# Kernel optimization log

Hardware: AMD Instinct MI355X
Metric: run time of the kernel (lower is better)

Reference implementation:

```python
import jax, jax.numpy as jnp
import numpy as np

# Model dims (match init_kwargs)
B, L, C = 4, 4096, 1024   # batch, seq_len, dim
M = 128                   # memory_dim
P = 4                     # n_persistent
S = 64                    # segment_size
H = 8                     # num_heads in nn.MultiheadAttention


def _ln(x, g, b, eps=1e-5):
    mu = jnp.mean(x, -1, keepdims=True)
    var = jnp.mean((x - mu) ** 2, -1, keepdims=True)
    return (x - mu) * jax.lax.rsqrt(var + eps) * g + b


def setup_inputs() -> dict:
    key = jax.random.key(0)
    ks = jax.random.split(key, 16)
    def n(k, shape, s=0.02):
        return jax.random.normal(k, shape, jnp.float32) * s
    return {
        "x": jax.random.normal(ks[0], (B, L, C), jnp.float32),
        "persistent_memory": n(ks[1], (1, P, C)),
        "Wq": n(ks[2], (C, C)),            # query_proj (no bias)
        "Wk": n(ks[3], (C, C)),            # key_proj (no bias)
        "Wv": n(ks[4], (C, C)),            # value_proj (no bias)
        # NeuralMemoryModule.memory_net: Linear(C->M), SiLU, LN(M), Linear(M->M), LN(M)
        "mem_W1": n(ks[5], (M, C)), "mem_b1": jnp.zeros((M,)),
        "mem_ln1_g": jnp.ones((M,)), "mem_ln1_b": jnp.zeros((M,)),
        "mem_W2": n(ks[6], (M, M)), "mem_b2": jnp.zeros((M,)),
        "mem_ln2_g": jnp.ones((M,)), "mem_ln2_b": jnp.zeros((M,)),
        "mem_out_W": n(ks[7], (C, M)), "mem_out_b": jnp.zeros((C,)),
        "memory_state": jnp.zeros((1, M)),  # persistent buffer (zeros at init)
        # nn.MultiheadAttention in/out projections
        "mha_Wq": n(ks[8], (C, C)), "mha_bq": jnp.zeros((C,)),
        "mha_Wk": n(ks[9], (C, C)), "mha_bk": jnp.zeros((C,)),
        "mha_Wv": n(ks[10], (C, C)), "mha_bv": jnp.zeros((C,)),
        "mha_Wo": n(ks[11], (C, C)), "mha_bo": jnp.zeros((C,)),
        "gn_g": jnp.ones((C,)), "gn_b": jnp.zeros((C,)),   # gate_norm
        "gate_W": n(ks[12], (C, C)), "gate_b": jnp.zeros((C,)),
        "out_W": n(ks[13], (C, C)), "out_b": jnp.zeros((C,)),
    }


def reference(x, persistent_memory, Wq, Wk, Wv,
              mem_W1, mem_b1, mem_ln1_g, mem_ln1_b,
              mem_W2, mem_b2, mem_ln2_g, mem_ln2_b,
              mem_out_W, mem_out_b, memory_state,
              mha_Wq, mha_bq, mha_Wk, mha_bk, mha_Wv, mha_bv, mha_Wo, mha_bo,
              gn_g, gn_b, gate_W, gate_b, out_W, out_b):
    Bx, Lx, Cx = x.shape
    n_seg = Lx // S
    # Eval-mode: memory_state is frozen, so all segments are independent ->
    # process every segment in parallel instead of a Python loop over L.
    xs = x.reshape(Bx * n_seg, S, Cx)           # [N, S, C]
    q_seg = xs @ Wq.T                            # query_proj
    # retrieve from long-term memory: memory_net(queries) + memory_state -> output_proj
    h = jax.nn.silu(q_seg @ mem_W1.T + mem_b1)
    h = _ln(h, mem_ln1_g, mem_ln1_b)
    h = h @ mem_W2.T + mem_b2
    h = _ln(h, mem_ln2_g, mem_ln2_b)             # [N, S, M]
    retrieved = (h + memory_state[0]) @ mem_out_W.T + mem_out_b  # [N, S, C]
    # context = [retrieved_memory, persistent_memory, current_segment]
    pm = jnp.broadcast_to(persistent_memory, (Bx * n_seg, P, Cx))
    context = jnp.concatenate([retrieved, pm, xs], axis=1)       # [N, T, C], T=S+P+S
    k_in = context @ Wk.T
    v_in = context @ Wv.T
    T = context.shape[1]
    hd = Cx // H
    q = (q_seg @ mha_Wq.T + mha_bq).reshape(-1, S, H, hd)
    k = (k_in @ mha_Wk.T + mha_bk).reshape(-1, T, H, hd)
    v = (v_in @ mha_Wv.T + mha_bv).reshape(-1, T, H, hd)
    scores = jnp.einsum('nshd,nthd->nhst', q, k) / jnp.sqrt(jnp.float32(hd))
    attn = jnp.einsum('nhst,nthd->nshd', jax.nn.softmax(scores, -1), v)
    attn = attn.reshape(-1, S, Cx) @ mha_Wo.T + mha_bo           # [N, S, C]
    # learned gate blend + output projection
    gate = jax.nn.sigmoid(_ln(attn, gn_g, gn_b) @ gate_W.T + gate_b)
    out = (gate * attn + xs) @ out_W.T + out_b
    return out.reshape(Bx, Lx, Cx)
```

## Files before the change

### kernel.cpp

```cpp
#include <hip/hip_runtime.h>
#include <hip/hip_bf16.h>
#include <math.h>


using bf16 = __hip_bfloat16;

typedef __attribute__((ext_vector_type(8))) short bf16x8;
typedef __attribute__((ext_vector_type(4))) float f32x4;

__device__ __forceinline__ float ldf(const bf16* p) { return __bfloat162float(*p); }
__device__ __forceinline__ float ldf(const float* p) { return *p; }
__device__ __forceinline__ void stf(bf16* p, float v) { *p = __float2bfloat16(v); }
__device__ __forceinline__ void stf(float* p, float v) { *p = v; }
__device__ __forceinline__ float b2f(const bf16& b) { return __bfloat162float(b); }
__device__ __forceinline__ float bsf(short s) {
  union { unsigned u; float f; } cv;
  cv.u = (unsigned)(unsigned short)s << 16;
  return cv.f;
}

enum { ACT_NONE = 0, ACT_SILU = 1, ACT_SIGMOID = 2, ACT_GATE = 3, ACT_PSILU = 4 };

__global__ void detect_kernel(const unsigned short* g, int* flag) {
  if (threadIdx.x == 0) *flag = (g[0] != 0) ? 1 : 0;
}

struct ConvArgs {
  const void* src[29];
  bf16* dst[29];
  int n[29];
  int bstart[30];
};

__global__ __launch_bounds__(256) void convall_kernel(ConvArgs a, const int* __restrict__ flag) {
  int b = blockIdx.x;
  int ti = 0;
  while (ti < 28 && b >= a.bstart[ti + 1]) ++ti;
  int i = (b - a.bstart[ti]) * 256 + threadIdx.x;
  if (i >= a.n[ti]) return;
  if (*flag) a.dst[ti][i] = ((const bf16*)a.src[ti])[i];
  else a.dst[ti][i] = __float2bfloat16(((const float*)a.src[ti])[i]);
}

__global__ __launch_bounds__(256) void conv_kernel(
    const void* __restrict__ src, bf16* __restrict__ dst, int n, size_t src_off,
    const int* __restrict__ flag) {
  int i = (blockIdx.x * 256 + threadIdx.x) * 8;
  if (i >= n) return;
  if (*flag) {
    *(uint4*)((unsigned short*)dst + i) =
        *(const uint4*)((const unsigned short*)src + src_off + i);
  } else {
    const float* s = (const float*)src + src_off + i;
    const float4 a = *(const float4*)s;
    const float4 b = *(const float4*)(s + 4);
    bf16 t[8] = {__float2bfloat16(a.x), __float2bfloat16(a.y),
                 __float2bfloat16(a.z), __float2bfloat16(a.w),
                 __float2bfloat16(b.x), __float2bfloat16(b.y),
                 __float2bfloat16(b.z), __float2bfloat16(b.w)};
    *(uint4*)((unsigned short*)dst + i) = *(const uint4*)t;
  }
}

__global__ __launch_bounds__(256) void pack_bias4(
    const bf16* __restrict__ bk, const bf16* __restrict__ bv,
    const bf16* __restrict__ bq, const bf16* __restrict__ b1,
    bf16* __restrict__ o) {
  int j = blockIdx.x * 256 + threadIdx.x;
  if (j >= 3200) return;
  float v;
  if (j < 1024) v = b2f(bk[j]);
  else if (j < 2048) v = b2f(bv[j - 1024]);
  else if (j < 3072) v = b2f(bq[j - 2048]);
  else v = b2f(b1[j - 3072]);
  o[j] = __float2bfloat16(v);
}

__global__ __launch_bounds__(256) void transpose_kernel(
    const bf16* __restrict__ srcb, bf16* __restrict__ dstb, int rows, int cols) {
  __shared__ unsigned short t[64][72];
  const unsigned short* src = (const unsigned short*)srcb;
  unsigned short* dst = (unsigned short*)dstb;
  const int r0 = blockIdx.y * 64, c0 = blockIdx.x * 64;
  for (int e = threadIdx.x; e < 64 * 8; e += 256) {
    int r = e >> 3, c8 = e & 7;
    uint4 v = *(const uint4*)(src + (size_t)(r0 + r) * cols + c0 + c8 * 8);
    *(uint4*)&t[r][c8 * 8] = v;
  }
  __syncthreads();
  for (int e = threadIdx.x; e < 64 * 8; e += 256) {
    int c = e >> 3, r8 = (e & 7) * 8;
    unsigned short v[8];
#pragma unroll
    for (int j = 0; j < 8; ++j) v[j] = t[r8 + j][c];
    *(uint4*)(dst + (size_t)(c0 + c) * rows + r0 + r8) = *(uint4*)v;
  }
}

__global__ __launch_bounds__(256) void kpvp_kernel(
    const bf16* __restrict__ pmb, const bf16* __restrict__ mobb,
    const bf16* __restrict__ Wb, const bf16* __restrict__ bias4b,
    bf16* __restrict__ kp, bf16* __restrict__ vp, bf16* __restrict__ bkv)
{
  const short* pm = (const short*)pmb;
  const short* mob = (const short*)mobb;
  const short* W = (const short*)Wb;
  const int wave = threadIdx.x >> 6, lane = threadIdx.x & 63;
  const int c = blockIdx.x * 4 + wave;
  const short* wrow = W + (size_t)c * 1024 + lane * 16;
  const bf16x8 w0 = *(const bf16x8*)wrow;
  const bf16x8 w1 = *(const bf16x8*)(wrow + 8);
  float acc[5];
#pragma unroll
  for (int m = 0; m < 5; ++m) {
    const short* prow = (m < 4) ? (pm + m * 1024 + lane * 16) : (mob + lane * 16);
    const bf16x8 p0 = *(const bf16x8*)prow;
    const bf16x8 p1 = *(const bf16x8*)(prow + 8);
    float s = 0.f;
#pragma unroll
    for (int j = 0; j < 8; ++j) s += bsf(w0[j]) * bsf(p0[j]) + bsf(w1[j]) * bsf(p1[j]);
    acc[m] = s;
  }
#pragma unroll
  for (int d = 1; d < 64; d <<= 1) {
#pragma unroll
    for (int m = 0; m < 5; ++m) acc[m] += __shfl_xor(acc[m], d);
  }
  if (lane == 0) {
    const float bv = b2f(bias4b[c]);
    bf16* dst = (c < 1024) ? (kp + c) : (vp + (c - 1024));
#pragma unroll
    for (int m = 0; m < 4; ++m) stf(dst + m * 1024, acc[m] + bv);
    stf(&bkv[c], acc[4] + bv);
  }
}

__device__ __forceinline__ void gl_lds16(const short* g, short* l) {
  __builtin_amdgcn_global_load_lds(
      (const __attribute__((address_space(1))) void*)g,
      (__attribute__((address_space(3))) void*)l, 16, 0, 0);
}

template <typename TC, int ACT, bool HAS_BIAS>
__global__ __launch_bounds__(256) void mgemm(
    const bf16* __restrict__ Ab, const bf16* __restrict__ Bw,
    const bf16* __restrict__ bias, TC* __restrict__ C,
    int M, int N, int K, int lda, int ldc,
    const bf16* __restrict__ ao, const void* __restrict__ xsrc, size_t xoff,
    const int* __restrict__ flag, int pn)
{
  __shared__ short As[2][128 * 32];
  __shared__ short Bs[2][128 * 32];
  const short* A = (const short*)Ab;
  const short* B = (const short*)Bw;
  const int tid = threadIdx.x;
  const int m0 = blockIdx.x * 128, n0 = blockIdx.y * 128;
  const int wave = tid >> 6, lane = tid & 63;
  const int wm = (wave & 1) * 64, wn = (wave >> 1) * 64;
  const int fm = lane & 15;
  const int fq = lane >> 4;
  const int fks = (fq ^ ((fm >> 1) & 3)) * 8;

  const int srow = tid >> 2;
  const int scol = ((tid & 3) ^ ((tid >> 3) & 3)) * 8;
  const short* gA0 = A + (size_t)(m0 + srow) * lda + scol;
  const short* gA1 = A + (size_t)(m0 + 64 + srow) * lda + scol;
  const short* gB0 = B + (size_t)(n0 + srow) * K + scol;
  const short* gB1 = B + (size_t)(n0 + 64 + srow) * K + scol;

  f32x4 acc[4][4] = {};
  const int NT = K >> 5;

#define STAGE(buf, k0)                              \
  do {                                              \
    gl_lds16(gA0 + (k0), &As[buf][tid * 8]);        \
    gl_lds16(gA1 + (k0), &As[buf][(256 + tid) * 8]);\
    gl_lds16(gB0 + (k0), &Bs[buf][tid * 8]);        \
    gl_lds16(gB1 + (k0), &Bs[buf][(256 + tid) * 8]);\
  } while (0)

  STAGE(0, 0);
  STAGE(1, 32);

  for (int kt = 0; kt < NT; ++kt) {
    const int cur = kt & 1;
    if (kt == NT - 1) asm volatile("s_waitcnt vmcnt(0)" ::: "memory");
    else              asm volatile("s_waitcnt vmcnt(4)" ::: "memory");
    __builtin_amdgcn_s_barrier();
    bf16x8 af[4], bfr[4];
#pragma unroll
    for (int i = 0; i < 4; ++i)
      af[i] = *(const bf16x8*)&As[cur][(wm + i * 16 + fm) * 32 + fks];
#pragma unroll
    for (int j = 0; j < 4; ++j)
      bfr[j] = *(const bf16x8*)&Bs[cur][(wn + j * 16 + fm) * 32 + fks];
#pragma unroll
    for (int i = 0; i < 4; ++i)
#pragma unroll
      for (int j = 0; j < 4; ++j)
        acc[i][j] = __builtin_amdgcn_mfma_f32_16x16x32_bf16(af[i], bfr[j], acc[i][j], 0, 0, 0);
    asm volatile("s_waitcnt lgkmcnt(0)" ::: "memory");
    __builtin_amdgcn_s_barrier();
    if (kt + 2 < NT) STAGE(cur, (kt + 2) * 32);
  }
#undef STAGE

  const int rg = fq * 4;
#pragma unroll
  for (int i = 0; i < 4; ++i) {
#pragma unroll
    for (int j = 0; j < 4; ++j) {
      const int n = n0 + wn + j * 16 + fm;
      float bv = 0.f;
      if (HAS_BIAS) bv = b2f(bias[n]);
#pragma unroll
      for (int r = 0; r < 4; ++r) {
        const int m = m0 + wm + i * 16 + rg + r;
        float v = acc[i][j][r] + bv;
        if (ACT == ACT_SILU) v = v / (1.f + __expf(-v));
        if (ACT == ACT_PSILU) { if (n >= pn) v = v / (1.f + __expf(-v)); }
        if (ACT == ACT_SIGMOID) v = 1.f / (1.f + __expf(-v));
        if (ACT == ACT_GATE) {
          v = 1.f / (1.f + __expf(-v));
          const size_t e = (size_t)m * 1024 + n;
          const float xv = *flag ? b2f(((const bf16*)xsrc)[xoff + e])
                                 : ((const float*)xsrc)[xoff + e];
          v = v * b2f(ao[e]) + xv;
        }
        stf(&C[(size_t)m * ldc + n], v);
      }
    }
  }
}

template <typename TC, int ACT, bool HAS_BIAS>
__global__ __launch_bounds__(512, 2) void tgemm(
    const bf16* __restrict__ Ab, const bf16* __restrict__ Bw,
    const bf16* __restrict__ bias, TC* __restrict__ C,
    int M, int N, int K, int lda, int ldc,
    const bf16* __restrict__ ao, const void* __restrict__ xsrc, size_t xoff,
    const int* __restrict__ flag, int pn)
{
  __shared__ short LA[3][256 * 64];
  __shared__ short LB[3][128 * 64];
  const short* A = (const short*)Ab;
  const short* B = (const short*)Bw;
  const int tid = threadIdx.x;
  const int m0 = blockIdx.x * 256, n0 = blockIdx.y * 128;
  const int wave = tid >> 6, lane = tid & 63;
  const int wm = (wave & 1) * 128;
  const int wn = (wave >> 1) * 32;
  const int fm = lane & 15;
  const int fq = lane >> 4;

  const int srowA = tid >> 3;
  const int sgrp = ((tid & 7) ^ ((tid >> 3) & 7)) * 8;
  const short* tA0 = A + (size_t)(m0 + srowA) * lda + sgrp;
  const short* tA1 = A + (size_t)(m0 + 64 + srowA) * lda + sgrp;
  const short* tA2 = A + (size_t)(m0 + 128 + srowA) * lda + sgrp;
  const short* tA3 = A + (size_t)(m0 + 192 + srowA) * lda + sgrp;
  const short* tB0 = B + (size_t)(n0 + srowA) * K + sgrp;
  const short* tB1 = B + (size_t)(n0 + 64 + srowA) * K + sgrp;

  f32x4 acc[8][2] = {};
  const int NT = K >> 6;

#define TSTAGE(buf, t)                                   \
  do {                                                   \
    const int k0_ = (t) * 64;                            \
    gl_lds16(tA0 + k0_, &LA[buf][tid * 8]);              \
    gl_lds16(tA1 + k0_, &LA[buf][4096 + tid * 8]);       \
    gl_lds16(tA2 + k0_, &LA[buf][8192 + tid * 8]);       \
    gl_lds16(tA3 + k0_, &LA[buf][12288 + tid * 8]);      \
    gl_lds16(tB0 + k0_, &LB[buf][tid * 8]);              \
    gl_lds16(tB1 + k0_, &LB[buf][4096 + tid * 8]);       \
  } while (0)

  TSTAGE(0, 0);
  TSTAGE(1, 1);
  asm volatile("s_waitcnt vmcnt(6)" ::: "memory");
  __builtin_amdgcn_s_barrier();

  for (int t = 0; t < NT; ++t) {
    const int buf = t % 3;
    if (t + 2 < NT) TSTAGE((t + 2) % 3, t + 2);
    const short* la = &LA[buf][0];
    const short* lb = &LB[buf][0];
#pragma unroll
    for (int kk = 0; kk < 2; ++kk) {
      const int sw = ((kk * 4 + fq) ^ (fm & 7)) * 8;
      bf16x8 af[8], bfr[2];
#pragma unroll
      for (int mi = 0; mi < 8; ++mi)
        af[mi] = *(const bf16x8*)&la[(wm + mi * 16 + fm) * 64 + sw];
#pragma unroll
      for (int nj = 0; nj < 2; ++nj)
        bfr[nj] = *(const bf16x8*)&lb[(wn + nj * 16 + fm) * 64 + sw];
      __builtin_amdgcn_s_setprio(1);
#pragma unroll
      for (int mi = 0; mi < 8; ++mi)
#pragma unroll
        for (int nj = 0; nj < 2; ++nj)
          acc[mi][nj] = __builtin_amdgcn_mfma_f32_16x16x32_bf16(af[mi], bfr[nj], acc[mi][nj], 0, 0, 0);
      __builtin_amdgcn_s_setprio(0);
    }
    if (t + 1 < NT) {
      if (t + 2 < NT) asm volatile("s_waitcnt vmcnt(6)" ::: "memory");
      else            asm volatile("s_waitcnt vmcnt(0)" ::: "memory");
      __builtin_amdgcn_s_barrier();
    }
  }
#undef TSTAGE

#pragma unroll
  for (int mi = 0; mi < 8; ++mi) {
#pragma unroll
    for (int nj = 0; nj < 2; ++nj) {
      const int n = n0 + wn + nj * 16 + fm;
      float bv = 0.f;
      if (HAS_BIAS) bv = b2f(bias[n]);
#pragma unroll
      for (int r = 0; r < 4; ++r) {
        const int m = m0 + wm + mi * 16 + fq * 4 + r;
        float v = acc[mi][nj][r] + bv;
        if (ACT == ACT_SILU) v = v / (1.f + __expf(-v));
        if (ACT == ACT_PSILU) { if (n >= pn) v = v / (1.f + __expf(-v)); }
        if (ACT == ACT_SIGMOID) v = 1.f / (1.f + __expf(-v));
        if (ACT == ACT_GATE) {
          v = 1.f / (1.f + __expf(-v));
          const size_t e = (size_t)m * 1024 + n;
          const float xv = *flag ? b2f(((const bf16*)xsrc)[xoff + e])
                                 : ((const float*)xsrc)[xoff + e];
          v = v * b2f(ao[e]) + xv;
        }
        stf(&C[(size_t)m * ldc + n], v);
      }
    }
  }
}

__global__ __launch_bounds__(256) void kgemm(
    const bf16* __restrict__ Ab, const bf16* __restrict__ Bw,
    float* __restrict__ P, int M, int N, int K, int lda)
{
  __shared__ short As[128 * 32];
  __shared__ short Bs[128 * 32];
  const short* A = (const short*)Ab;
  const short* B = (const short*)Bw;
  const int tid = threadIdx.x;
  const int m0 = blockIdx.x * 128, n0 = blockIdx.y * 128;
  const int kb = blockIdx.z * (K >> 2), ke = kb + (K >> 2);
  const int wave = tid >> 6, lane = tid & 63;
  const int wm = (wave & 1) * 64, wn = (wave >> 1) * 64;
  const int fm = lane & 15;
  const int fk = (lane >> 4) * 8;

  const int srow = tid >> 2, scol = (tid & 3) * 8;
  const short* gA0 = A + (size_t)(m0 + srow) * lda + scol;
  const short* gA1 = A + (size_t)(m0 + 64 + srow) * lda + scol;
  const short* gB0 = B + (size_t)(n0 + srow) * K + scol;
  const short* gB1 = B + (size_t)(n0 + 64 + srow) * K + scol;
  short* lA0 = As + tid * 8;
  short* lA1 = As + (256 + tid) * 8;
  short* lB0 = Bs + tid * 8;
  short* lB1 = Bs + (256 + tid) * 8;

  f32x4 acc[4][4] = {};

  for (int k0 = kb; k0 < ke; k0 += 32) {
    gl_lds16(gA0 + k0, lA0);
    gl_lds16(gA1 + k0, lA1);
    gl_lds16(gB0 + k0, lB0);
    gl_lds16(gB1 + k0, lB1);
    __syncthreads();
    bf16x8 af[4], bfr[4];
#pragma unroll
    for (int i = 0; i < 4; ++i)
      af[i] = *(const bf16x8*)&As[(wm + i * 16 + fm) * 32 + fk];
#pragma unroll
    for (int j = 0; j < 4; ++j)
      bfr[j] = *(const bf16x8*)&Bs[(wn + j * 16 + fm) * 32 + fk];
#pragma unroll
    for (int i = 0; i < 4; ++i)
#pragma unroll
      for (int j = 0; j < 4; ++j)
        acc[i][j] = __builtin_amdgcn_mfma_f32_16x16x32_bf16(af[i], bfr[j], acc[i][j], 0, 0, 0);
    __syncthreads();
  }

  float* Cp = P + (size_t)blockIdx.z * ((size_t)M * N);
  const int rg = (lane >> 4) * 4;
#pragma unroll
  for (int i = 0; i < 4; ++i)
#pragma unroll
    for (int j = 0; j < 4; ++j) {
      const int n = n0 + wn + j * 16 + fm;
#pragma unroll
      for (int r = 0; r < 4; ++r) {
        const int m = m0 + wm + i * 16 + rg + r;
        Cp[(size_t)m * N + n] = acc[i][j][r];
      }
    }
}

__global__ __launch_bounds__(256) void foldfin_kernel(
    const float* __restrict__ P, bf16* __restrict__ o, int MN) {
  int i = blockIdx.x * 256 + threadIdx.x;
  if (i >= MN) return;
  float s = P[i] + P[i + (size_t)MN] + P[i + 2 * (size_t)MN] + P[i + 3 * (size_t)MN];
  o[i] = __float2bfloat16(s);
}

template <typename TI, typename TO, bool ADD, int W, int BS>
__global__ __launch_bounds__(BS) void ln_kernel(
    const TI* __restrict__ in, const bf16* __restrict__ g, const bf16* __restrict__ b,
    const bf16* __restrict__ addv, TO* __restrict__ out, int ldin)
{
  __shared__ float red[BS];
  const int row = blockIdx.x;
  const TI* rin = in + (size_t)row * ldin;
  TO* rout = out + (size_t)row * W;
  const int NP = W / BS;
  float v[NP];
  float s = 0.f;
#pragma unroll
  for (int i = 0; i < NP; ++i) { v[i] = ldf(&rin[threadIdx.x + i * BS]); s += v[i]; }
  red[threadIdx.x] = s; __syncthreads();
  for (int o = BS / 2; o > 0; o >>= 1) {
    if (threadIdx.x < o) red[threadIdx.x] += red[threadIdx.x + o];
    __syncthreads();
  }
  const float mean = red[0] / W;
  __syncthreads();
  float sq = 0.f;
#pragma unroll
  for (int i = 0; i < NP; ++i) { float d = v[i] - mean; sq += d * d; }
  red[threadIdx.x] = sq; __syncthreads();
  for (int o = BS / 2; o > 0; o >>= 1) {
    if (threadIdx.x < o) red[threadIdx.x] += red[threadIdx.x + o];
    __syncthreads();
  }
  const float rstd = rsqrtf(red[0] / W + 1e-5f);
#pragma unroll
  for (int i = 0; i < NP; ++i) {
    int c = threadIdx.x + i * BS;
    float o_ = (v[i] - mean) * rstd * b2f(g[c]) + b2f(b[c]);
    if (ADD) o_ += b2f(addv[c]);
    stf(&rout[c], o_);
  }
}

__global__ __launch_bounds__(512) void attn_kernel(
    const bf16* __restrict__ qg, int str_q,
    const bf16* __restrict__ krv, int str_r,
    const bf16* __restrict__ kxv, int str_x, const bf16* __restrict__ kpg,
    const bf16* __restrict__ vpg, bf16* __restrict__ outg)
{
  __shared__ short qs[4 * 64 * 32];
  __shared__ short ksl[4 * 144 * 32];
  __shared__ short vt[128 * 168];
  __shared__ short pl[64 * 168];

  const int tid = threadIdx.x;
  unsigned bid = blockIdx.x;
  {
    const unsigned nwg = gridDim.x;
    const unsigned q_ = nwg >> 3, r_ = nwg & 7;
    const unsigned xcd = bid & 7, loc = bid >> 3;
    bid = (xcd < r_ ? xcd * (q_ + 1) : r_ * (q_ + 1) + (xcd - r_) * q_) + loc;
  }
  const int seg = (int)(bid >> 3), h = (int)(bid & 7);
  const unsigned short* q = (const unsigned short*)qg + (size_t)seg * 64 * str_q + h * 128;
  const unsigned short* kv_r = (const unsigned short*)krv + (size_t)seg * 64 * str_r + h * 128;
  const unsigned short* kv_x = (const unsigned short*)kxv + (size_t)seg * 64 * str_x + h * 128;
  const unsigned short* kp = (const unsigned short*)kpg;
  const unsigned short* vp = (const unsigned short*)vpg;
  const size_t obase = (size_t)seg * 64 * 1024 + h * 128;

  for (int ch = tid; ch < 64 * 16; ch += 512) {
    int row = ch >> 4, k8 = ch & 15;
    uint4 v = *(const uint4*)(q + (size_t)row * str_q + k8 * 8);
    *(uint4*)&qs[((k8 >> 2) * 64 + row) * 32 + (k8 & 3) * 8] = v;
  }
  for (int ch = tid; ch < 132 * 16; ch += 512) {
    int t = ch >> 4, k8 = ch & 15;
    const unsigned short* src;
    if (t < 64) src = kv_r + (size_t)t * str_r;
    else if (t < 68) src = kp + (size_t)(t - 64) * 1024 + h * 128;
    else src = kv_x + (size_t)(t - 68) * str_x;
    uint4 v = *(const uint4*)(src + k8 * 8);
    *(uint4*)&ksl[((k8 >> 2) * 144 + t) * 32 + (k8 & 3) * 8] = v;
  }
  __syncthreads();

  const int wave = tid >> 6, lane = tid & 63;
  const int fm = lane & 15, fq = lane >> 4;

  if (wave < 4) {
    const int s0 = wave * 16;
    f32x4 acc[10];
#pragma unroll
    for (int tt = 0; tt < 10; ++tt) acc[tt] = (f32x4){0.f, 0.f, 0.f, 0.f};
#pragma unroll
    for (int kb = 0; kb < 4; ++kb) {
      const bf16x8 a = *(const bf16x8*)&qs[(kb * 64 + s0 + fm) * 32 + fq * 8];
#pragma unroll
      for (int tt = 0; tt < 9; ++tt) {
        const bf16x8 b = *(const bf16x8*)&ksl[(kb * 144 + tt * 16 + fm) * 32 + fq * 8];
        acc[tt] = __builtin_amdgcn_mfma_f32_16x16x32_bf16(a, b, acc[tt], 0, 0, 0);
      }
    }
    const float scale = 0.08838834764831845f;
#pragma unroll
    for (int r = 0; r < 4; ++r) {
      float m = -3.0e38f;
#pragma unroll
      for (int tt = 0; tt < 9; ++tt) {
        int t = tt * 16 + fm;
        if (t < 132) m = fmaxf(m, acc[tt][r] * scale);
      }
      for (int d = 1; d < 16; d <<= 1) m = fmaxf(m, __shfl_xor(m, d));
      float e[10];
      float sum = 0.f;
#pragma unroll
      for (int tt = 0; tt < 10; ++tt) {
        int t = tt * 16 + fm;
        float ev = 0.f;
        if (t < 132) ev = __expf(acc[tt][r] * scale - m);
        e[tt] = ev; sum += ev;
      }
      for (int d = 1; d < 16; d <<= 1) sum += __shfl_xor(sum, d);
      const float inv = 1.f / sum;
      const int s = s0 + fq * 4 + r;
#pragma unroll
      for (int tt = 0; tt < 10; ++tt) {
        bf16 pv = __float2bfloat16(e[tt] * inv);
        pl[s * 168 + tt * 16 + fm] = *(const short*)&pv;
      }
    }
  } else {
    for (int ch = tid - 256; ch < 132 * 32; ch += 256) {
      int t = ch >> 5, d4 = (ch & 31) * 4;
      const unsigned short* src;
      if (t < 64) src = kv_r + 1024 + (size_t)t * str_r;
      else if (t < 68) src = vp + (size_t)(t - 64) * 1024 + h * 128;
      else src = kv_x + 1024 + (size_t)(t - 68) * str_x;
      uint2 w = *(const uint2*)(src + d4);
      vt[(d4 + 0) * 168 + t] = (short)(w.x & 0xffffu);
      vt[(d4 + 1) * 168 + t] = (short)(w.x >> 16);
      vt[(d4 + 2) * 168 + t] = (short)(w.y & 0xffffu);
      vt[(d4 + 3) * 168 + t] = (short)(w.y >> 16);
    }
    for (int ch = tid - 256; ch < 128 * 32; ch += 256) {
      int d = ch >> 5, tp = 132 + (ch & 31);
      vt[d * 168 + tp] = 0;
    }
  }
  __syncthreads();

  const int dt = wave;
  bf16x8 af[5];
#pragma unroll
  for (int kb = 0; kb < 5; ++kb)
    af[kb] = *(const bf16x8*)&vt[(dt * 16 + fm) * 168 + kb * 32 + fq * 8];
#pragma unroll
  for (int st = 0; st < 4; ++st) {
    f32x4 o = (f32x4){0.f, 0.f, 0.f, 0.f};
#pragma unroll
    for (int kb = 0; kb < 5; ++kb) {
      const bf16x8 bp = *(const bf16x8*)&pl[(st * 16 + fm) * 168 + kb * 32 + fq * 8];
      o = __builtin_amdgcn_mfma_f32_16x16x32_bf16(af[kb], bp, o, 0, 0, 0);
    }
    const int s = st * 16 + fm;
    bf16 b0 = __float2bfloat16(o[0]), b1 = __float2bfloat16(o[1]);
    bf16 b2 = __float2bfloat16(o[2]), b3 = __float2bfloat16(o[3]);
    uint2 w;
    w.x = ((unsigned)(*(unsigned short*)&b1) << 16) | (*(unsigned short*)&b0);
    w.y = ((unsigned)(*(unsigned short*)&b3) << 16) | (*(unsigned short*)&b2);
    *(uint2*)((unsigned short*)outg + obase + (size_t)s * 1024 + dt * 16 + fq * 4) = w;
  }
}

extern "C" void kernel_launch(void* const* d_in, const int* in_sizes, int n_in,
                              void* d_out, int out_size, void* d_ws, size_t ws_size,
                              hipStream_t stream)
{
  (void)n_in; (void)out_size;
  const int R = 16384, Cd = 1024;

  char* ws = (char*)d_ws;
  size_t off = 0;
  auto alloc = [&](size_t bytes) -> void* {
    void* p = ws + off;
    off += (bytes + 255) & ~(size_t)255;
    return p;
  };

  int* flag = (int*)alloc(256);
  bf16* W4    = (bf16*)alloc((size_t)3200 * Cd * sizeof(bf16));
  bf16* bias4 = (bf16*)alloc(3200 * sizeof(bf16));
  bf16* T     = (bf16*)alloc((size_t)Cd * Cd * sizeof(bf16));
  bf16* Wc    = (bf16*)alloc((size_t)2048 * 128 * sizeof(bf16));
  bf16* kp    = (bf16*)alloc((size_t)4 * Cd * sizeof(bf16));
  bf16* vp    = (bf16*)alloc((size_t)4 * Cd * sizeof(bf16));
  bf16* bkv   = (bf16*)alloc(2048 * sizeof(bf16));
  bf16* WqStk = (bf16*)alloc((size_t)1152 * Cd * sizeof(bf16));
  bf16* nb[30];
  nb[0] = nullptr;
  for (int i = 1; i < 30; ++i) nb[i] = (bf16*)alloc((size_t)in_sizes[i] * sizeof(bf16));
  nb[16] = WqStk;
  nb[5]  = WqStk + (size_t)1024 * Cd;
  const size_t fixed_end = off;

  size_t avail = (ws_size > fixed_end + (1u << 20)) ? (ws_size - fixed_end - (1u << 20)) : 0;
  int crmax = (int)(avail / 17152);
  if (crmax > R) crmax = R;
  if (crmax < 128) crmax = 128;
  int nch = (R + crmax - 1) / crmax;
  int CR = ((R / nch + 127) / 128) * 128;
  while (CR * nch < R) CR += 128;

  const size_t chunk_start = off;
  const size_t RB = (size_t)CR * Cd * sizeof(bf16);
  bf16* Xc  = (bf16*)alloc(RB);
  bf16* QS4 = (bf16*)alloc((size_t)CR * 3200 * sizeof(bf16));
  bf16* h1b = (bf16*)alloc((size_t)CR * 128 * sizeof(bf16));
  bf16* h2b = (bf16*)alloc((size_t)CR * 128 * sizeof(bf16));
  bf16* Bb  = (bf16*)alloc(RB);
  bf16* KVr = (bf16*)alloc(2 * RB);
  bf16* Cc  = (bf16*)alloc(RB);
  const size_t chunk_bytes = off - chunk_start;

  dim3 blk(256);
  auto g128 = [](int M_, int N_) { return dim3((unsigned)(M_ / 128), (unsigned)(N_ / 128)); };
  auto g256 = [](int M_, int N_) { return dim3((unsigned)(M_ / 256), (unsigned)(N_ / 128)); };

  detect_kernel<<<1, 64, 0, stream>>>((const unsigned short*)d_in[24], flag);
  {
    ConvArgs a;
    int bs = 0;
    for (int i = 1; i < 30; ++i) {
      a.src[i - 1] = d_in[i];
      a.dst[i - 1] = nb[i];
      a.n[i - 1] = in_sizes[i];
      a.bstart[i - 1] = bs;
      bs += (in_sizes[i] + 255) / 256;
    }
    a.bstart[29] = bs;
    convall_kernel<<<dim3((unsigned)bs), blk, 0, stream>>>(a, flag);
  }
  const bf16 *pm = nb[1], *Wq = nb[2], *Wk = nb[3], *Wv = nb[4];
  const bf16 *mem_W1 = nb[5], *mem_b1 = nb[6], *ln1g = nb[7], *ln1b = nb[8];
  const bf16 *mem_W2 = nb[9], *mem_b2 = nb[10], *ln2g = nb[11], *ln2b = nb[12];
  const bf16 *mem_oW = nb[13], *mem_ob = nb[14], *mstate = nb[15];
  const bf16 *mhaWq = nb[16], *mhabq = nb[17], *mhaWk = nb[18], *mhabk = nb[19];
  const bf16 *mhaWv = nb[20], *mhabv = nb[21], *mhaWo = nb[22], *mhabo = nb[23];
  const bf16 *gn_g = nb[24], *gn_b = nb[25], *gateW = nb[26], *gateb = nb[27];
  const bf16 *outW = nb[28], *outb = nb[29];
  bf16* Wkk = W4;
  bf16* Wvv = W4 + (size_t)1024 * Cd;
  bf16* Wqq = W4 + (size_t)2048 * Cd;
  bf16* Wm1 = W4 + (size_t)3072 * Cd;

  const bool use_ks = chunk_bytes >= (size_t)4 * 1152 * 1024 * sizeof(float);
  if (use_ks) {
    float* P = (float*)Xc;
    transpose_kernel<<<dim3(16, 16), blk, 0, stream>>>(Wq, T, 1024, 1024);
    kgemm<<<dim3(9, 8, 4), blk, 0, stream>>>(WqStk, T, P, 1152, 1024, 1024, 1024);
    foldfin_kernel<<<dim3(4608), blk, 0, stream>>>(P, Wqq, 1152 * 1024);
    transpose_kernel<<<dim3(16, 16), blk, 0, stream>>>(Wk, T, 1024, 1024);
    kgemm<<<dim3(8, 8, 4), blk, 0, stream>>>(mhaWk, T, P, 1024, 1024, 1024, 1024);
    foldfin_kernel<<<dim3(4096), blk, 0, stream>>>(P, Wkk, 1024 * 1024);
    transpose_kernel<<<dim3(16, 16), blk, 0, stream>>>(Wv, T, 1024, 1024);
    kgemm<<<dim3(8, 8, 4), blk, 0, stream>>>(mhaWv, T, P, 1024, 1024, 1024, 1024);
    foldfin_kernel<<<dim3(4096), blk, 0, stream>>>(P, Wvv, 1024 * 1024);
    transpose_kernel<<<dim3(2, 16), blk, 0, stream>>>(mem_oW, T, 1024, 128);
    kgemm<<<dim3(16, 1, 4), blk, 0, stream>>>(W4, T, P, 2048, 128, 1024, 1024);
    foldfin_kernel<<<dim3(1024), blk, 0, stream>>>(P, Wc, 2048 * 128);
  } else {
    transpose_kernel<<<dim3(16, 16), blk, 0, stream>>>(Wq, T, 1024, 1024);
    mgemm<bf16, ACT_NONE, false><<<g128(1024, 1024), blk, 0, stream>>>(
        mhaWq, T, nullptr, Wqq, 1024, 1024, 1024, 1024, 1024, nullptr, nullptr, 0, nullptr, 0);
    mgemm<bf16, ACT_NONE, false><<<g128(128, 1024), blk, 0, stream>>>(
        mem_W1, T, nullptr, Wm1, 128, 1024, 1024, 1024, 1024, nullptr, nullptr, 0, nullptr, 0);
    transpose_kernel<<<dim3(16, 16), blk, 0, stream>>>(Wk, T, 1024, 1024);
    mgemm<bf16, ACT_NONE, false><<<g128(1024, 1024), blk, 0, stream>>>(
        mhaWk, T, nullptr, Wkk, 1024, 1024, 1024, 1024, 1024, nullptr, nullptr, 0, nullptr, 0);
    transpose_kernel<<<dim3(16, 16), blk, 0, stream>>>(Wv, T, 1024, 1024);
    mgemm<bf16, ACT_NONE, false><<<g128(1024, 1024), blk, 0, stream>>>(
        mhaWv, T, nullptr, Wvv, 1024, 1024, 1024, 1024, 1024, nullptr, nullptr, 0, nullptr, 0);
    transpose_kernel<<<dim3(2, 16), blk, 0, stream>>>(mem_oW, T, 1024, 128);
    mgemm<bf16, ACT_NONE, false><<<g128(2048, 128), blk, 0, stream>>>(
        W4, T, nullptr, Wc, 2048, 128, 1024, 1024, 128, nullptr, nullptr, 0, nullptr, 0);
  }
  pack_bias4<<<13, blk, 0, stream>>>(mhabk, mhabv, mhabq, mem_b1, bias4);
  kpvp_kernel<<<dim3(512), blk, 0, stream>>>(pm, mem_ob, W4, bias4, kp, vp, bkv);

  for (int r0 = 0; r0 < R; r0 += CR) {
    const int cr = (R - r0 < CR) ? (R - r0) : CR;
    const int n = cr * Cd;
    const bool big = (cr % 256) == 0;
    conv_kernel<<<dim3((n / 8 + 255) / 256), blk, 0, stream>>>(
        d_in[0], Xc, n, (size_t)r0 * Cd, flag);

    if (big)
      tgemm<bf16, ACT_PSILU, true><<<g256(cr, 3200), dim3(512), 0, stream>>>(
          Xc, W4, bias4, QS4, cr, 3200, 1024, 1024, 3200, nullptr, nullptr, 0, nullptr, 3072);
    else
      mgemm<bf16, ACT_PSILU, true><<<g128(cr, 3200), blk, 0, stream>>>(
          Xc, W4, bias4, QS4, cr, 3200, 1024, 1024, 3200, nullptr, nullptr, 0, nullptr, 3072);

    ln_kernel<bf16, bf16, false, 128, 128><<<cr, 128, 0, stream>>>(
        QS4 + 3072, ln1g, ln1b, nullptr, h2b, 3200);
    mgemm<bf16, ACT_NONE, true><<<g128(cr, 128), blk, 0, stream>>>(
        h2b, mem_W2, mem_b2, h1b, cr, 128, 128, 128, 128, nullptr, nullptr, 0, nullptr, 0);
    ln_kernel<bf16, bf16, true, 128, 128><<<cr, 128, 0, stream>>>(h1b, ln2g, ln2b, mstate, h2b, 128);
    mgemm<bf16, ACT_NONE, true><<<g128(cr, 2048), blk, 0, stream>>>(
        h2b, Wc, bkv, KVr, cr, 2048, 128, 128, 2048, nullptr, nullptr, 0, nullptr, 0);

    attn_kernel<<<dim3((cr / 64) * 8), dim3(512), 0, stream>>>(
        QS4 + 2048, 3200, KVr, 2048, QS4, 3200, kp, vp, Xc);

    if (big)
      tgemm<bf16, ACT_NONE, true><<<g256(cr, Cd), dim3(512), 0, stream>>>(
          Xc, mhaWo, mhabo, Bb, cr, Cd, Cd, Cd, Cd, nullptr, nullptr, 0, nullptr, 0);
    else
      mgemm<bf16, ACT_NONE, true><<<g128(cr, Cd), blk, 0, stream>>>(
          Xc, mhaWo, mhabo, Bb, cr, Cd, Cd, Cd, Cd, nullptr, nullptr, 0, nullptr, 0);
    ln_kernel<bf16, bf16, false, 1024, 256><<<cr, 256, 0, stream>>>(Bb, gn_g, gn_b, nullptr, Cc, Cd);
    if (big) {
      tgemm<bf16, ACT_GATE, true><<<g256(cr, Cd), dim3(512), 0, stream>>>(
          Cc, gateW, gateb, Xc, cr, Cd, Cd, Cd, Cd, Bb, d_in[0], (size_t)r0 * Cd, flag, 0);
      tgemm<float, ACT_NONE, true><<<g256(cr, Cd), dim3(512), 0, stream>>>(
          Xc, outW, outb, (float*)d_out + (size_t)r0 * Cd, cr, Cd, Cd, Cd, Cd,
          nullptr, nullptr, 0, nullptr, 0);
    } else {
      mgemm<bf16, ACT_GATE, true><<<g128(cr, Cd), blk, 0, stream>>>(
          Cc, gateW, gateb, Xc, cr, Cd, Cd, Cd, Cd, Bb, d_in[0], (size_t)r0 * Cd, flag, 0);
      mgemm<float, ACT_NONE, true><<<g128(cr, Cd), blk, 0, stream>>>(
          Xc, outW, outb, (float*)d_out + (size_t)r0 * Cd, cr, Cd, Cd, Cd, Cd,
          nullptr, nullptr, 0, nullptr, 0);
    }
  }
}
```

Baseline: 878.3 us.

## Rework 256x128 GEMM into ping-pong schedule with split staging and square wave tiles

Replaces the tgemm kernel with pgemm. Each wave now owns a 64x64 sub-tile (4x4 MFMAs) instead of 128x32, which balances A and B fragment loads from shared memory. Global-to-LDS staging for the next tile is split across the two k-halves, with barriers between them so memory and MFMA phases interleave across waves, in the style of a ping-pong schedule. Launch bounds drop to 1 block per CU, which allows more registers but lowers occupancy and relies on the explicit barriers to hide latency.

After: 828.6 us. 1.06x faster.

```diff
diff --git a/kernel.cpp b/kernel.cpp
--- a/kernel.cpp
+++ b/kernel.cpp
@@ -234,7 +234,7 @@
 }
 
 template <typename TC, int ACT, bool HAS_BIAS>
-__global__ __launch_bounds__(512, 2) void tgemm(
+__global__ __launch_bounds__(512, 1) void pgemm(
     const bf16* __restrict__ Ab, const bf16* __restrict__ Bw,
     const bf16* __restrict__ bias, TC* __restrict__ C,
     int M, int N, int K, int lda, int ldc,
@@ -248,81 +248,111 @@
   const int tid = threadIdx.x;
   const int m0 = blockIdx.x * 256, n0 = blockIdx.y * 128;
   const int wave = tid >> 6, lane = tid & 63;
-  const int wm = (wave & 1) * 128;
-  const int wn = (wave >> 1) * 32;
+  const int wm = (wave >> 1) * 64;
+  const int wn = (wave & 1) * 64;
   const int fm = lane & 15;
   const int fq = lane >> 4;
-
-  const int srowA = tid >> 3;
-  const int sgrp = ((tid & 7) ^ ((tid >> 3) & 7)) * 8;
-  const short* tA0 = A + (size_t)(m0 + srowA) * lda + sgrp;
-  const short* tA1 = A + (size_t)(m0 + 64 + srowA) * lda + sgrp;
-  const short* tA2 = A + (size_t)(m0 + 128 + srowA) * lda + sgrp;
-  const short* tA3 = A + (size_t)(m0 + 192 + srowA) * lda + sgrp;
-  const short* tB0 = B + (size_t)(n0 + srowA) * K + sgrp;
-  const short* tB1 = B + (size_t)(n0 + 64 + srowA) * K + sgrp;
-
-  f32x4 acc[8][2] = {};
+  const int swz = fm & 7;
+
+  const int srow = tid >> 3;
+  const int sgrp = ((tid & 7) ^ (srow & 7)) * 8;
+  const short* tA0 = A + (size_t)(m0 + srow) * lda + sgrp;
+  const short* tA1 = A + (size_t)(m0 + 64 + srow) * lda + sgrp;
+  const short* tA2 = A + (size_t)(m0 + 128 + srow) * lda + sgrp;
+  const short* tA3 = A + (size_t)(m0 + 192 + srow) * lda + sgrp;
+  const short* tB0 = B + (size_t)(n0 + srow) * K + sgrp;
+  const short* tB1 = B + (size_t)(n0 + 64 + srow) * K + sgrp;
+
+  f32x4 acc[4][4] = {};
   const int NT = K >> 6;
 
-#define TSTAGE(buf, t)                                   \
-  do {                                                   \
-    const int k0_ = (t) * 64;                            \
-    gl_lds16(tA0 + k0_, &LA[buf][tid * 8]);              \
-    gl_lds16(tA1 + k0_, &LA[buf][4096 + tid * 8]);       \
-    gl_lds16(tA2 + k0_, &LA[buf][8192 + tid * 8]);       \
-    gl_lds16(tA3 + k0_, &LA[buf][12288 + tid * 8]);      \
-    gl_lds16(tB0 + k0_, &LB[buf][tid * 8]);              \
-    gl_lds16(tB1 + k0_, &LB[buf][4096 + tid * 8]);       \
+#define PSTG0(buf, k0)                                \
+  do {                                                \
+    gl_lds16(tA0 + (k0), &LA[buf][tid * 8]);          \
+    gl_lds16(tA1 + (k0), &LA[buf][4096 + tid * 8]);   \
+    gl_lds16(tA2 + (k0), &LA[buf][8192 + tid * 8]);   \
   } while (0)
-
-  TSTAGE(0, 0);
-  TSTAGE(1, 1);
+#define PSTG1(buf, k0)                                \
+  do {                                                \
+    gl_lds16(tA3 + (k0), &LA[buf][12288 + tid * 8]);  \
+    gl_lds16(tB0 + (k0), &LB[buf][tid * 8]);          \
+    gl_lds16(tB1 + (k0), &LB[buf][4096 + tid * 8]);   \
+  } while (0)
+
+  PSTG0(0, 0);  PSTG1(0, 0);
+  PSTG0(1, 64); PSTG1(1, 64);
   asm volatile("s_waitcnt vmcnt(6)" ::: "memory");
   __builtin_amdgcn_s_barrier();
 
   for (int t = 0; t < NT; ++t) {
     const int buf = t % 3;
-    if (t + 2 < NT) TSTAGE((t + 2) % 3, t + 2);
+    const int nbuf = (t + 2) % 3;
+    const bool stg = (t + 2) < NT;
     const short* la = &LA[buf][0];
     const short* lb = &LB[buf][0];
-#pragma unroll
-    for (int kk = 0; kk < 2; ++kk) {
-      const int sw = ((kk * 4 + fq) ^ (fm & 7)) * 8;
-      bf16x8 af[8], bfr[2];
-#pragma unroll
-      for (int mi = 0; mi < 8; ++mi)
-        af[mi] = *(const bf16x8*)&la[(wm + mi * 16 + fm) * 64 + sw];
-#pragma unroll
-      for (int nj = 0; nj < 2; ++nj)
-        bfr[nj] = *(const bf16x8*)&lb[(wn + nj * 16 + fm) * 64 + sw];
+    const int k2 = (t + 2) * 64;
+
+    {
+      bf16x8 af[4], bfr[4];
+      const int sw = (fq ^ swz) * 8;
+#pragma unroll
+      for (int i = 0; i < 4; ++i)
+        af[i] = *(const bf16x8*)&la[(wm + i * 16 + fm) * 64 + sw];
+#pragma unroll
+      for (int j = 0; j < 4; ++j)
+        bfr[j] = *(const bf16x8*)&lb[(wn + j * 16 + fm) * 64 + sw];
+      if (stg) PSTG0(nbuf, k2);
+      __builtin_amdgcn_s_barrier();
+      asm volatile("s_waitcnt lgkmcnt(0)" ::: "memory");
       __builtin_amdgcn_s_setprio(1);
 #pragma unroll
-      for (int mi = 0; mi < 8; ++mi)
-#pragma unroll
-        for (int nj = 0; nj < 2; ++nj)
-          acc[mi][nj] = __builtin_amdgcn_mfma_f32_16x16x32_bf16(af[mi], bfr[nj], acc[mi][nj], 0, 0, 0);
+      for (int i = 0; i < 4; ++i)
+#pragma unroll
+        for (int j = 0; j < 4; ++j)
+          acc[i][j] = __builtin_amdgcn_mfma_f32_16x16x32_bf16(af[i], bfr[j], acc[i][j], 0, 0, 0);
       __builtin_amdgcn_s_setprio(0);
-    }
-    if (t + 1 < NT) {
-      if (t + 2 < NT) asm volatile("s_waitcnt vmcnt(6)" ::: "memory");
-      else            asm volatile("s_waitcnt vmcnt(0)" ::: "memory");
       __builtin_amdgcn_s_barrier();
     }
-  }
-#undef TSTAGE
-
-#pragma unroll
-  for (int mi = 0; mi < 8; ++mi) {
-#pragma unroll
-    for (int nj = 0; nj < 2; ++nj) {
-      const int n = n0 + wn + nj * 16 + fm;
+    {
+      bf16x8 af[4], bfr[4];
+      const int sw = ((4 + fq) ^ swz) * 8;
+#pragma unroll
+      for (int i = 0; i < 4; ++i)
+        af[i] = *(const bf16x8*)&la[(wm + i * 16 + fm) * 64 + sw];
+#pragma unroll
+      for (int j = 0; j < 4; ++j)
+        bfr[j] = *(const bf16x8*)&lb[(wn + j * 16 + fm) * 64 + sw];
+      if (stg) PSTG1(nbuf, k2);
+      __builtin_amdgcn_s_barrier();
+      asm volatile("s_waitcnt lgkmcnt(0)" ::: "memory");
+      __builtin_amdgcn_s_setprio(1);
+#pragma unroll
+      for (int i = 0; i < 4; ++i)
+#pragma unroll
+        for (int j = 0; j < 4; ++j)
+          acc[i][j] = __builtin_amdgcn_mfma_f32_16x16x32_bf16(af[i], bfr[j], acc[i][j], 0, 0, 0);
+      __builtin_amdgcn_s_setprio(0);
+      if (t + 1 < NT) {
+        if (stg) asm volatile("s_waitcnt vmcnt(6)" ::: "memory");
+        else     asm volatile("s_waitcnt vmcnt(0)" ::: "memory");
+      }
+      __builtin_amdgcn_s_barrier();
+    }
+  }
+#undef PSTG0
+#undef PSTG1
+
+#pragma unroll
+  for (int i = 0; i < 4; ++i) {
+#pragma unroll
+    for (int j = 0; j < 4; ++j) {
+      const int n = n0 + wn + j * 16 + fm;
       float bv = 0.f;
       if (HAS_BIAS) bv = b2f(bias[n]);
 #pragma unroll
       for (int r = 0; r < 4; ++r) {
-        const int m = m0 + wm + mi * 16 + fq * 4 + r;
-        float v = acc[mi][nj][r] + bv;
+        const int m = m0 + wm + i * 16 + fq * 4 + r;
+        float v = acc[i][j][r] + bv;
         if (ACT == ACT_SILU) v = v / (1.f + __expf(-v));
         if (ACT == ACT_PSILU) { if (n >= pn) v = v / (1.f + __expf(-v)); }
         if (ACT == ACT_SIGMOID) v = 1.f / (1.f + __expf(-v));
@@ -704,7 +734,7 @@
         d_in[0], Xc, n, (size_t)r0 * Cd, flag);
 
     if (big)
-      tgemm<bf16, ACT_PSILU, true><<<g256(cr, 3200), dim3(512), 0, stream>>>(
+      pgemm<bf16, ACT_PSILU, true><<<g256(cr, 3200), dim3(512), 0, stream>>>(
           Xc, W4, bias4, QS4, cr, 3200, 1024, 1024, 3200, nullptr, nullptr, 0, nullptr, 3072);
     else
       mgemm<bf16, ACT_PSILU, true><<<g128(cr, 3200), blk, 0, stream>>>(
@@ -722,16 +752,16 @@
         QS4 + 2048, 3200, KVr, 2048, QS4, 3200, kp, vp, Xc);
 
     if (big)
-      tgemm<bf16, ACT_NONE, true><<<g256(cr, Cd), dim3(512), 0, stream>>>(
+      pgemm<bf16, ACT_NONE, true><<<g256(cr, Cd), dim3(512), 0, stream>>>(
           Xc, mhaWo, mhabo, Bb, cr, Cd, Cd, Cd, Cd, nullptr, nullptr, 0, nullptr, 0);
     else
       mgemm<bf16, ACT_NONE, true><<<g128(cr, Cd), blk, 0, stream>>>(
           Xc, mhaWo, mhabo, Bb, cr, Cd, Cd, Cd, Cd, nullptr, nullptr, 0, nullptr, 0);
     ln_kernel<bf16, bf16, false, 1024, 256><<<cr, 256, 0, stream>>>(Bb, gn_g, gn_b, nullptr, Cc, Cd);
     if (big) {
-      tgemm<bf16, ACT_GATE, true><<<g256(cr, Cd), dim3(512), 0, stream>>>(
+      pgemm<bf16, ACT_GATE, true><<<g256(cr, Cd), dim3(512), 0, stream>>>(
           Cc, gateW, gateb, Xc, cr, Cd, Cd, Cd, Cd, Bb, d_in[0], (size_t)r0 * Cd, flag, 0);
-      tgemm<float, ACT_NONE, true><<<g256(cr, Cd), dim3(512), 0, stream>>>(
+      pgemm<float, ACT_NONE, true><<<g256(cr, Cd), dim3(512), 0, stream>>>(
           Xc, outW, outb, (float*)d_out + (size_t)r0 * Cd, cr, Cd, Cd, Cd, Cd,
           nullptr, nullptr, 0, nullptr, 0);
     } else {
```

## Replace tgemm with 256x256-tile qgemm using split-K-half double buffering

Applied to the files above, without the earlier changes.

Replaces the 256x128 triple-buffered GEMM with a 256x256 tile kernel. Each K step is split into two 32-wide halves, and loads for the next tile are interleaved with MFMA sub-phases. The fused QKV/mem projection width is padded from 3200 to 3328 so it divides by 256, with zeroed padding weights and bias. This raises arithmetic intensity per tile and overlaps global-to-LDS loads with compute. In exchange it drops to one block per CU, does extra padded work, and adds more barriers per K step.

New measurement: 1.051 ms. 1.2x slower.

```diff
diff --git a/kernel.cpp b/kernel.cpp
--- a/kernel.cpp
+++ b/kernel.cpp
@@ -62,17 +62,22 @@
   }
 }
 
+__global__ __launch_bounds__(256) void zerobf_kernel(bf16* __restrict__ p, int n) {
+  int i = blockIdx.x * 256 + threadIdx.x;
+  if (i < n) p[i] = __float2bfloat16(0.f);
+}
+
 __global__ __launch_bounds__(256) void pack_bias4(
     const bf16* __restrict__ bk, const bf16* __restrict__ bv,
     const bf16* __restrict__ bq, const bf16* __restrict__ b1,
     bf16* __restrict__ o) {
   int j = blockIdx.x * 256 + threadIdx.x;
-  if (j >= 3200) return;
-  float v;
+  if (j >= 3328) return;
+  float v = 0.f;
   if (j < 1024) v = b2f(bk[j]);
   else if (j < 2048) v = b2f(bv[j - 1024]);
   else if (j < 3072) v = b2f(bq[j - 2048]);
-  else v = b2f(b1[j - 3072]);
+  else if (j < 3200) v = b2f(b1[j - 3072]);
   o[j] = __float2bfloat16(v);
 }
 
@@ -234,88 +239,97 @@
 }
 
 template <typename TC, int ACT, bool HAS_BIAS>
-__global__ __launch_bounds__(512, 2) void tgemm(
+__global__ __launch_bounds__(512, 1) void qgemm(
     const bf16* __restrict__ Ab, const bf16* __restrict__ Bw,
     const bf16* __restrict__ bias, TC* __restrict__ C,
     int M, int N, int K, int lda, int ldc,
     const bf16* __restrict__ ao, const void* __restrict__ xsrc, size_t xoff,
     const int* __restrict__ flag, int pn)
 {
-  __shared__ short LA[3][256 * 64];
-  __shared__ short LB[3][128 * 64];
+  __shared__ short LA[2][2][256 * 32];
+  __shared__ short LB[2][2][256 * 32];
   const short* A = (const short*)Ab;
   const short* B = (const short*)Bw;
   const int tid = threadIdx.x;
-  const int m0 = blockIdx.x * 256, n0 = blockIdx.y * 128;
+  const int m0 = blockIdx.x * 256, n0 = blockIdx.y * 256;
   const int wave = tid >> 6, lane = tid & 63;
   const int wm = (wave & 1) * 128;
-  const int wn = (wave >> 1) * 32;
+  const int wn = (wave >> 1) * 64;
   const int fm = lane & 15;
   const int fq = lane >> 4;
-
-  const int srowA = tid >> 3;
-  const int sgrp = ((tid & 7) ^ ((tid >> 3) & 7)) * 8;
-  const short* tA0 = A + (size_t)(m0 + srowA) * lda + sgrp;
-  const short* tA1 = A + (size_t)(m0 + 64 + srowA) * lda + sgrp;
-  const short* tA2 = A + (size_t)(m0 + 128 + srowA) * lda + sgrp;
-  const short* tA3 = A + (size_t)(m0 + 192 + srowA) * lda + sgrp;
-  const short* tB0 = B + (size_t)(n0 + srowA) * K + sgrp;
-  const short* tB1 = B + (size_t)(n0 + 64 + srowA) * K + sgrp;
-
-  f32x4 acc[8][2] = {};
+  const int grp = (fq ^ ((fm >> 1) & 3)) * 8;
+
+  const int srow = tid >> 2;
+  const int sg = ((tid & 3) ^ ((tid >> 3) & 3)) * 8;
+  const short* aS0 = A + (size_t)(m0 + srow) * lda + sg;
+  const short* aS1 = A + (size_t)(m0 + 128 + srow) * lda + sg;
+  const short* bS0 = B + (size_t)(n0 + srow) * K + sg;
+  const short* bS1 = B + (size_t)(n0 + 128 + srow) * K + sg;
+
+  f32x4 acc[8][4] = {};
   const int NT = K >> 6;
 
-#define TSTAGE(buf, t)                                   \
-  do {                                                   \
-    const int k0_ = (t) * 64;                            \
-    gl_lds16(tA0 + k0_, &LA[buf][tid * 8]);              \
-    gl_lds16(tA1 + k0_, &LA[buf][4096 + tid * 8]);       \
-    gl_lds16(tA2 + k0_, &LA[buf][8192 + tid * 8]);       \
-    gl_lds16(tA3 + k0_, &LA[buf][12288 + tid * 8]);      \
-    gl_lds16(tB0 + k0_, &LB[buf][tid * 8]);              \
-    gl_lds16(tB1 + k0_, &LB[buf][4096 + tid * 8]);       \
+#define QSTG(b, t, h)                                     \
+  do {                                                    \
+    const int ks_ = (t) * 64 + (h) * 32;                  \
+    gl_lds16(aS0 + ks_, &LA[b][h][tid * 8]);              \
+    gl_lds16(aS1 + ks_, &LA[b][h][4096 + tid * 8]);       \
+    gl_lds16(bS0 + ks_, &LB[b][h][tid * 8]);              \
+    gl_lds16(bS1 + ks_, &LB[b][h][4096 + tid * 8]);       \
   } while (0)
 
-  TSTAGE(0, 0);
-  TSTAGE(1, 1);
-  asm volatile("s_waitcnt vmcnt(6)" ::: "memory");
+  QSTG(0, 0, 0);
+  QSTG(0, 0, 1);
+  asm volatile("s_waitcnt vmcnt(4)" ::: "memory");
   __builtin_amdgcn_s_barrier();
 
+  bf16x8 af[8], bf[2];
+
   for (int t = 0; t < NT; ++t) {
-    const int buf = t % 3;
-    if (t + 2 < NT) TSTAGE((t + 2) % 3, t + 2);
-    const short* la = &LA[buf][0];
-    const short* lb = &LB[buf][0];
-#pragma unroll
-    for (int kk = 0; kk < 2; ++kk) {
-      const int sw = ((kk * 4 + fq) ^ (fm & 7)) * 8;
-      bf16x8 af[8], bfr[2];
-#pragma unroll
-      for (int mi = 0; mi < 8; ++mi)
-        af[mi] = *(const bf16x8*)&la[(wm + mi * 16 + fm) * 64 + sw];
-#pragma unroll
-      for (int nj = 0; nj < 2; ++nj)
-        bfr[nj] = *(const bf16x8*)&lb[(wn + nj * 16 + fm) * 64 + sw];
-      __builtin_amdgcn_s_setprio(1);
-#pragma unroll
-      for (int mi = 0; mi < 8; ++mi)
-#pragma unroll
-        for (int nj = 0; nj < 2; ++nj)
-          acc[mi][nj] = __builtin_amdgcn_mfma_f32_16x16x32_bf16(af[mi], bfr[nj], acc[mi][nj], 0, 0, 0);
-      __builtin_amdgcn_s_setprio(0);
-    }
-    if (t + 1 < NT) {
-      if (t + 2 < NT) asm volatile("s_waitcnt vmcnt(6)" ::: "memory");
-      else            asm volatile("s_waitcnt vmcnt(0)" ::: "memory");
-      __builtin_amdgcn_s_barrier();
-    }
-  }
-#undef TSTAGE
+    const int c = t & 1, s = c ^ 1;
+    const bool nx = (t + 1) < NT;
+#pragma unroll
+    for (int h = 0; h < 2; ++h) {
+#pragma unroll
+      for (int njp = 0; njp < 2; ++njp) {
+        const short* la = &LA[c][h][0];
+        const short* lb = &LB[c][h][0];
+        if (njp == 0) {
+#pragma unroll
+          for (int mi = 0; mi < 8; ++mi)
+            af[mi] = *(const bf16x8*)&la[(wm + mi * 16 + fm) * 32 + grp];
+        }
+#pragma unroll
+        for (int j = 0; j < 2; ++j)
+          bf[j] = *(const bf16x8*)&lb[(wn + (njp * 2 + j) * 16 + fm) * 32 + grp];
+        if (h == 0 && nx) QSTG(s, t + 1, njp);
+        __builtin_amdgcn_s_barrier();
+        asm volatile("s_waitcnt lgkmcnt(0)" ::: "memory");
+        __builtin_amdgcn_sched_barrier(0);
+        __builtin_amdgcn_s_setprio(1);
+#pragma unroll
+        for (int mi = 0; mi < 8; ++mi)
+#pragma unroll
+          for (int j = 0; j < 2; ++j)
+            acc[mi][njp * 2 + j] = __builtin_amdgcn_mfma_f32_16x16x32_bf16(
+                af[mi], bf[j], acc[mi][njp * 2 + j], 0, 0, 0);
+        __builtin_amdgcn_s_setprio(0);
+        if (h == 0 && njp == 1) {
+          if (nx) asm volatile("s_waitcnt vmcnt(8)" ::: "memory");
+          else    asm volatile("s_waitcnt vmcnt(0)" ::: "memory");
+        }
+        if (h == 1 && njp == 1 && nx)
+          asm volatile("s_waitcnt vmcnt(4)" ::: "memory");
+        __builtin_amdgcn_s_barrier();
+      }
+    }
+  }
+#undef QSTG
 
 #pragma unroll
   for (int mi = 0; mi < 8; ++mi) {
 #pragma unroll
-    for (int nj = 0; nj < 2; ++nj) {
+    for (int nj = 0; nj < 4; ++nj) {
       const int n = n0 + wn + nj * 16 + fm;
       float bv = 0.f;
       if (HAS_BIAS) bv = b2f(bias[n]);
@@ -587,6 +601,7 @@
 {
   (void)n_in; (void)out_size;
   const int R = 16384, Cd = 1024;
+  const int NP4 = 3328;
 
   char* ws = (char*)d_ws;
   size_t off = 0;
@@ -597,8 +612,8 @@
   };
 
   int* flag = (int*)alloc(256);
-  bf16* W4    = (bf16*)alloc((size_t)3200 * Cd * sizeof(bf16));
-  bf16* bias4 = (bf16*)alloc(3200 * sizeof(bf16));
+  bf16* W4    = (bf16*)alloc((size_t)NP4 * Cd * sizeof(bf16));
+  bf16* bias4 = (bf16*)alloc(NP4 * sizeof(bf16));
   bf16* T     = (bf16*)alloc((size_t)Cd * Cd * sizeof(bf16));
   bf16* Wc    = (bf16*)alloc((size_t)2048 * 128 * sizeof(bf16));
   bf16* kp    = (bf16*)alloc((size_t)4 * Cd * sizeof(bf16));
@@ -613,17 +628,17 @@
   const size_t fixed_end = off;
 
   size_t avail = (ws_size > fixed_end + (1u << 20)) ? (ws_size - fixed_end - (1u << 20)) : 0;
-  int crmax = (int)(avail / 17152);
+  int crmax = (int)(avail / 17408);
   if (crmax > R) crmax = R;
-  if (crmax < 128) crmax = 128;
+  if (crmax < 256) crmax = 256;
   int nch = (R + crmax - 1) / crmax;
-  int CR = ((R / nch + 127) / 128) * 128;
-  while (CR * nch < R) CR += 128;
+  int CR = ((R / nch + 255) / 256) * 256;
+  while (CR * nch < R) CR += 256;
 
   const size_t chunk_start = off;
   const size_t RB = (size_t)CR * Cd * sizeof(bf16);
   bf16* Xc  = (bf16*)alloc(RB);
-  bf16* QS4 = (bf16*)alloc((size_t)CR * 3200 * sizeof(bf16));
+  bf16* QS4 = (bf16*)alloc((size_t)CR * NP4 * sizeof(bf16));
   bf16* h1b = (bf16*)alloc((size_t)CR * 128 * sizeof(bf16));
   bf16* h2b = (bf16*)alloc((size_t)CR * 128 * sizeof(bf16));
   bf16* Bb  = (bf16*)alloc(RB);
@@ -633,7 +648,7 @@
 
   dim3 blk(256);
   auto g128 = [](int M_, int N_) { return dim3((unsigned)(M_ / 128), (unsigned)(N_ / 128)); };
-  auto g256 = [](int M_, int N_) { return dim3((unsigned)(M_ / 256), (unsigned)(N_ / 128)); };
+  auto g256 = [](int M_, int N_) { return dim3((unsigned)(M_ / 256), (unsigned)(N_ / 256)); };
 
   detect_kernel<<<1, 64, 0, stream>>>((const unsigned short*)d_in[24], flag);
   {
@@ -661,6 +676,8 @@
   bf16* Wvv = W4 + (size_t)1024 * Cd;
   bf16* Wqq = W4 + (size_t)2048 * Cd;
   bf16* Wm1 = W4 + (size_t)3072 * Cd;
+
+  zerobf_kernel<<<dim3(512), blk, 0, stream>>>(W4 + (size_t)3200 * Cd, 128 * Cd);
 
   const bool use_ks = chunk_bytes >= (size_t)4 * 1152 * 1024 * sizeof(float);
   if (use_ks) {
@@ -704,14 +721,14 @@
         d_in[0], Xc, n, (size_t)r0 * Cd, flag);
 
     if (big)
-      tgemm<bf16, ACT_PSILU, true><<<g256(cr, 3200), dim3(512), 0, stream>>>(
-          Xc, W4, bias4, QS4, cr, 3200, 1024, 1024, 3200, nullptr, nullptr, 0, nullptr, 3072);
+      qgemm<bf16, ACT_PSILU, true><<<g256(cr, NP4), dim3(512), 0, stream>>>(
+          Xc, W4, bias4, QS4, cr, NP4, 1024, 1024, NP4, nullptr, nullptr, 0, nullptr, 3072);
     else
-      mgemm<bf16, ACT_PSILU, true><<<g128(cr, 3200), blk, 0, stream>>>(
-          Xc, W4, bias4, QS4, cr, 3200, 1024, 1024, 3200, nullptr, nullptr, 0, nullptr, 3072);
+      mgemm<bf16, ACT_PSILU, true><<<g128(cr, NP4), blk, 0, stream>>>(
+          Xc, W4, bias4, QS4, cr, NP4, 1024, 1024, NP4, nullptr, nullptr, 0, nullptr, 3072);
 
     ln_kernel<bf16, bf16, false, 128, 128><<<cr, 128, 0, stream>>>(
-        QS4 + 3072, ln1g, ln1b, nullptr, h2b, 3200);
+        QS4 + 3072, ln1g, ln1b, nullptr, h2b, NP4);
     mgemm<bf16, ACT_NONE, true><<<g128(cr, 128), blk, 0, stream>>>(
         h2b, mem_W2, mem_b2, h1b, cr, 128, 128, 128, 128, nullptr, nullptr, 0, nullptr, 0);
     ln_kernel<bf16, bf16, true, 128, 128><<<cr, 128, 0, stream>>>(h1b, ln2g, ln2b, mstate, h2b, 128);
@@ -719,19 +736,19 @@
         h2b, Wc, bkv, KVr, cr, 2048, 128, 128, 2048, nullptr, nullptr, 0, nullptr, 0);
 
     attn_kernel<<<dim3((cr / 64) * 8), dim3(512), 0, stream>>>(
-        QS4 + 2048, 3200, KVr, 2048, QS4, 3200, kp, vp, Xc);
+        QS4 + 2048, NP4, KVr, 2048, QS4, NP4, kp, vp, Xc);
 
     if (big)
-      tgemm<bf16, ACT_NONE, true><<<g256(cr, Cd), dim3(512), 0, stream>>>(
+      qgemm<bf16, ACT_NONE, true><<<g256(cr, Cd), dim3(512), 0, stream>>>(
           Xc, mhaWo, mhabo, Bb, cr, Cd, Cd, Cd, Cd, nullptr, nullptr, 0, nullptr, 0);
     else
       mgemm<bf16, ACT_NONE, true><<<g128(cr, Cd), blk, 0, stream>>>(
           Xc, mhaWo, mhabo, Bb, cr, Cd, Cd, Cd, Cd, nullptr, nullptr, 0, nullptr, 0);
     ln_kernel<bf16, bf16, false, 1024, 256><<<cr, 256, 0, stream>>>(Bb, gn_g, gn_b, nullptr, Cc, Cd);
     if (big) {
-      tgemm<bf16, ACT_GATE, true><<<g256(cr, Cd), dim3(512), 0, stream>>>(
+      qgemm<bf16, ACT_GATE, true><<<g256(cr, Cd), dim3(512), 0, stream>>>(
           Cc, gateW, gateb, Xc, cr, Cd, Cd, Cd, Cd, Bb, d_in[0], (size_t)r0 * Cd, flag, 0);
-      tgemm<float, ACT_NONE, true><<<g256(cr, Cd), dim3(512), 0, stream>>>(
+      qgemm<float, ACT_NONE, true><<<g256(cr, Cd), dim3(512), 0, stream>>>(
           Xc, outW, outb, (float*)d_out + (size_t)r0 * Cd, cr, Cd, Cd, Cd, Cd,
           nullptr, nullptr, 0, nullptr, 0);
     } else {
```
